# Kernel optimization log

Measured on AMD Instinct MI355X. Metric: run time of the kernel, lower is better.

The kernel has to match this reference:

```python
import jax, jax.numpy as jnp
import numpy as np
from jax import lax

GAMMA = 0.1  # fixed RBF bandwidth from LearnableRBFInfluence


def setup_inputs() -> dict:
    key = jax.random.key(0)
    k1, k2, k3, k4 = jax.random.split(key, 4)
    B, H, W = 2, 256, 256
    NUM_FILTERS, KS, NUM_BASIS = 48, 7, 31
    u_log = jax.random.normal(k1, (B, 1, H, W), jnp.float32)
    f_log = jax.random.normal(k2, (B, 1, H, W), jnp.float32)
    filters = jax.random.normal(k3, (NUM_FILTERS, 1, KS, KS), jnp.float32) * 0.05
    rbf_weights = jax.random.normal(k4, (NUM_FILTERS, NUM_BASIS), jnp.float32) * 0.05
    lambda_param = jnp.float32(0.1)
    return {"u_log": u_log, "f_log": f_log, "filters": filters,
            "rbf_weights": rbf_weights, "lambda_param": lambda_param}


def reference(u_log, f_log, filters, rbf_weights, lambda_param):
    # Batched form of the per-filter loop:
    #   conv[i] = conv2d(u, k_i)  ->  one grouped conv with 48 output channels
    num_basis = rbf_weights.shape[1]
    mu = jnp.linspace(-1.0, 1.0, num_basis).astype(u_log.dtype)  # [K]

    dn = lax.conv_dimension_numbers(u_log.shape, filters.shape, ('NCHW', 'OIHW', 'NCHW'))
    conv = lax.conv_general_dilated(u_log, filters, (1, 1), 'SAME',
                                    dimension_numbers=dn)  # [B,48,H,W]

    # RBF influence, per filter channel c: phi = sum_k w[c,k] * exp(-(conv-mu_k)^2/(2 g^2))
    diff = conv[..., None] - mu                              # [B,48,H,W,K]
    rbf = jnp.exp(-(diff * diff) / (2.0 * GAMMA * GAMMA))
    phi = jnp.einsum('bchwk,ck->bchw', rbf, rbf_weights)     # [B,48,H,W]

    # Per-filter conv2d(phi_i, flip(k_i)) summed over i == single conv
    # with OIHW weight [1,48,7,7] built from spatially-flipped filters.
    kT = jnp.flip(filters, axis=(2, 3)).transpose(1, 0, 2, 3)  # [1,48,7,7]
    dn2 = lax.conv_dimension_numbers(phi.shape, kT.shape, ('NCHW', 'OIHW', 'NCHW'))
    diffusion = lax.conv_general_dilated(phi, kT, (1, 1), 'SAME',
                                         dimension_numbers=dn2)  # [B,1,H,W]

    reaction = lambda_param * (u_log - f_log)
    return u_log - diffusion - reaction
```

## Files before the change

kernel.cpp:

```cpp
#include <hip/hip_runtime.h>

#define HH 256
#define WW 256
#define NPIX (2 * HH * WW)
#define NC 48
#define NB 31
#define NG 6
#define CG 8
#define OT 32
#define PT 38
#define PSTR 44
#define UT 44
#define USTR 52
#define TP 192

__global__ __launch_bounds__(256)
void tnrd_table(const float* __restrict__ wr, float2* __restrict__ tab)
{
    const int ch = blockIdx.x;
    const float* rc = wr + ch * NB;
    for (int j = threadIdx.x; j < TP; j += 256) {
        float v0 = 0.f, v1 = 0.f;
        float x0 = fmaf((float)j, 1.0f / 64.0f, -1.5f);
        float x1 = x0 + 1.0f / 64.0f;
        #pragma unroll
        for (int k = 0; k < NB; ++k) {
            float mu = -1.f + (float)k * (1.f / 15.f);
            float d0 = x0 - mu, d1 = x1 - mu;
            float w = rc[k];
            v0 = fmaf(w, __expf(-50.f * d0 * d0), v0);
            v1 = fmaf(w, __expf(-50.f * d1 * d1), v1);
        }
        tab[ch * TP + j] = make_float2(v0, v1 - v0);
    }
}

__global__ __launch_bounds__(256, 3)
void tnrd_main(const float* __restrict__ u,
               const float* __restrict__ wf,
               const float2* __restrict__ tab,
               float* __restrict__ part)
{
    __shared__ __align__(16) float u_s[UT * USTR];
    __shared__ __align__(16) float phi_s[4][PT * PSTR];

    const int tid = threadIdx.x;
    const int bx = blockIdx.x, by = blockIdx.y;
    const int b = blockIdx.z / NG, g = blockIdx.z % NG;
    const int c0g = g * CG;

    const int uy0 = by * OT - 6, ux0 = bx * OT - 6;
    const float* ub = u + b * (HH * WW);
    for (int i = tid; i < UT * USTR; i += 256) {
        int r = i / USTR, c = i - r * USTR;
        int gy = uy0 + r, gx = ux0 + c;
        float v = 0.f;
        if (c < UT && (unsigned)gy < HH && (unsigned)gx < WW)
            v = ub[gy * WW + gx];
        u_s[i] = v;
    }
    __syncthreads();

    const int oy = tid >> 3;
    const int ox0 = (tid & 7) * 4;
    float o0 = 0.f, o1 = 0.f, o2 = 0.f, o3 = 0.f;
    const int py0 = by * OT - 3, px0 = bx * OT - 3;

    auto conv1_pass = [&](int cp, float* __restrict__ bufA,
                          float* __restrict__ bufB) {
        const float* wA = wf + (c0g + 2 * cp) * 49;
        const float* wB = wA + 49;
        const float2* tA = tab + (c0g + 2 * cp) * TP;
        const float2* tB = tA + TP;
        for (int p = 0; p < 2; ++p) {
            const int gi = tid + p * 256;
            if (gi < PT * 10) {
                const int pr = gi % PT, pc = (gi / PT) * 4;
                float a0 = 0.f, a1 = 0.f, a2 = 0.f, a3 = 0.f;
                float b0 = 0.f, b1 = 0.f, b2 = 0.f, b3 = 0.f;
                const float* bptr = &u_s[pr * USTR + pc];

                auto fmab = [&](const float* wa, const float* wb,
                                float4 q0, float4 q1, float4 q2) {
                    float sv[12] = {q0.x, q0.y, q0.z, q0.w,
                                    q1.x, q1.y, q1.z, q1.w,
                                    q2.x, q2.y, q2.z, q2.w};
                    #pragma unroll
                    for (int dx = 0; dx < 7; ++dx) {
                        float fa = wa[dx], fb = wb[dx];
                        a0 = fmaf(sv[dx],     fa, a0);
                        a1 = fmaf(sv[dx + 1], fa, a1);
                        a2 = fmaf(sv[dx + 2], fa, a2);
                        a3 = fmaf(sv[dx + 3], fa, a3);
                        b0 = fmaf(sv[dx],     fb, b0);
                        b1 = fmaf(sv[dx + 1], fb, b1);
                        b2 = fmaf(sv[dx + 2], fb, b2);
                        b3 = fmaf(sv[dx + 3], fb, b3);
                    }
                };

                float4 c0 = *(const float4*)(bptr);
                float4 c1 = *(const float4*)(bptr + 4);
                float4 c2 = *(const float4*)(bptr + 8);
                #pragma unroll 1
                for (int dy = 0; dy < 6; ++dy) {
                    const float* nr = bptr + (dy + 1) * USTR;
                    float4 n0 = *(const float4*)(nr);
                    float4 n1 = *(const float4*)(nr + 4);
                    float4 n2 = *(const float4*)(nr + 8);
                    fmab(wA + dy * 7, wB + dy * 7, c0, c1, c2);
                    c0 = n0; c1 = n1; c2 = n2;
                }
                fmab(wA + 42, wB + 42, c0, c1, c2);

                const int gy = py0 + pr;
                const bool rowok = (unsigned)gy < HH;
                float av[4] = {a0, a1, a2, a3};
                float bv[4] = {b0, b1, b2, b3};
                float pha[4], phb[4];
                #pragma unroll
                for (int j = 0; j < 4; ++j) {
                    bool ok = rowok && (unsigned)(px0 + pc + j) < WW;
                    float ta = fminf(fmaxf(fmaf(av[j], 64.f, 96.f), 0.f), 191.999f);
                    float fja = floorf(ta);
                    float2 ea = tA[(int)fja];
                    float va = fmaf(ta - fja, ea.y, ea.x);
                    float tb = fminf(fmaxf(fmaf(bv[j], 64.f, 96.f), 0.f), 191.999f);
                    float fjb = floorf(tb);
                    float2 eb = tB[(int)fjb];
                    float vb = fmaf(tb - fjb, eb.y, eb.x);
                    pha[j] = ok ? va : 0.f;
                    phb[j] = ok ? vb : 0.f;
                }
                float* dA = bufA + pr * PSTR + pc;
                float* dB = bufB + pr * PSTR + pc;
                #pragma unroll
                for (int j = 0; j < 4; ++j) dA[j] = pha[j];
                #pragma unroll
                for (int j = 0; j < 4; ++j) dB[j] = phb[j];
            }
        }
    };

    conv1_pass(0, phi_s[0], phi_s[1]);
    __syncthreads();

    #pragma unroll 1
    for (int pass = 0; pass < 4; ++pass) {
        if (pass < 3) {
            const int nb_ = (pass + 1) & 1;
            conv1_pass(pass + 1, phi_s[2 * nb_], phi_s[2 * nb_ + 1]);
        }

        const float* wA = wf + (c0g + 2 * pass) * 49;
        const float* wB = wA + 49;
        const float* pA = phi_s[2 * (pass & 1)];
        const float* pB = phi_s[2 * (pass & 1) + 1];
        for (int dy = 0; dy < 7; ++dy) {
            const float* rA = pA + (oy + dy) * PSTR + ox0;
            const float* rB = pB + (oy + dy) * PSTR + ox0;
            float sa[10], sb[10];
            #pragma unroll
            for (int j = 0; j < 10; ++j) sa[j] = rA[j];
            #pragma unroll
            for (int j = 0; j < 10; ++j) sb[j] = rB[j];
            #pragma unroll
            for (int dx = 0; dx < 7; ++dx) {
                float fa = wA[(6 - dy) * 7 + (6 - dx)];
                float fb = wB[(6 - dy) * 7 + (6 - dx)];
                o0 = fmaf(sa[dx],     fa, o0);
                o1 = fmaf(sa[dx + 1], fa, o1);
                o2 = fmaf(sa[dx + 2], fa, o2);
                o3 = fmaf(sa[dx + 3], fa, o3);
                o0 = fmaf(sb[dx],     fb, o0);
                o1 = fmaf(sb[dx + 1], fb, o1);
                o2 = fmaf(sb[dx + 2], fb, o2);
                o3 = fmaf(sb[dx + 3], fb, o3);
            }
        }
        if (pass < 3) __syncthreads();
    }

    const int gy = by * OT + oy, gx = bx * OT + ox0;
    float4 v4 = make_float4(o0, o1, o2, o3);
    *reinterpret_cast<float4*>(part + (size_t)g * NPIX + b * (HH * WW)
                               + gy * WW + gx) = v4;
}

__global__ __launch_bounds__(256)
void combine_kernel(const float* __restrict__ u,
                    const float* __restrict__ f,
                    const float* __restrict__ lam,
                    const float* __restrict__ part,
                    float* __restrict__ out)
{
    int i = blockIdx.x * 256 + threadIdx.x;
    float d = 0.f;
    #pragma unroll
    for (int g = 0; g < NG; ++g) d += part[g * NPIX + i];
    float lv = lam[0];
    float uv = u[i];
    float fv = f[i];
    out[i] = uv - d - lv * (uv - fv);
}

extern "C" void kernel_launch(void* const* d_in, const int* in_sizes, int n_in,
                              void* d_out, int out_size, void* d_ws, size_t ws_size,
                              hipStream_t stream) {
    const float* u    = (const float*)d_in[0];
    const float* f    = (const float*)d_in[1];
    const float* filt = (const float*)d_in[2];
    const float* rbfw = (const float*)d_in[3];
    const float* lam  = (const float*)d_in[4];
    float* out = (float*)d_out;
    float* part = (float*)d_ws;
    float2* tabg = (float2*)d_out;

    tnrd_table<<<NC, 256, 0, stream>>>(rbfw, tabg);
    tnrd_main<<<dim3(8, 8, 2 * NG), 256, 0, stream>>>(u, filt, tabg, part);
    combine_kernel<<<512, 256, 0, stream>>>(u, f, lam, part, out);
}
```

Before: 110.5 us.

## Fuse RBF table build into main kernel with LDS table and vectorized LDS loads

Removes the separate table kernel launch. Each block now builds the RBF lookup table for its 8 channels in shared memory, using phi_s as scratch, and the LERP lookups read from LDS instead of global memory. The conv1 and conv2 inner loops are rewritten with float4/float2 LDS loads and manually unrolled macros, with vectorized float4 stores of phi. The cost is redundant table computation in every block (768 blocks each doing roughly 1544 points times 31 exps) and extra LDS usage that may reduce occupancy.

```diff
diff --git a/kernel.cpp b/kernel.cpp
--- a/kernel.cpp
+++ b/kernel.cpp
@@ -14,35 +14,46 @@
 #define USTR 52
 #define TP 192
 
-__global__ __launch_bounds__(256)
-void tnrd_table(const float* __restrict__ wr, float2* __restrict__ tab)
-{
-    const int ch = blockIdx.x;
-    const float* rc = wr + ch * NB;
-    for (int j = threadIdx.x; j < TP; j += 256) {
-        float v0 = 0.f, v1 = 0.f;
-        float x0 = fmaf((float)j, 1.0f / 64.0f, -1.5f);
-        float x1 = x0 + 1.0f / 64.0f;
-        #pragma unroll
-        for (int k = 0; k < NB; ++k) {
-            float mu = -1.f + (float)k * (1.f / 15.f);
-            float d0 = x0 - mu, d1 = x1 - mu;
-            float w = rc[k];
-            v0 = fmaf(w, __expf(-50.f * d0 * d0), v0);
-            v1 = fmaf(w, __expf(-50.f * d1 * d1), v1);
-        }
-        tab[ch * TP + j] = make_float2(v0, v1 - v0);
-    }
-}
+
+#define F1STEP(WI, s0, s1, s2, s3)                                      \
+    { float fa = wa[WI], fb = wb[WI];                                   \
+      a0 = fmaf(s0, fa, a0); a1 = fmaf(s1, fa, a1);                     \
+      a2 = fmaf(s2, fa, a2); a3 = fmaf(s3, fa, a3);                     \
+      b0 = fmaf(s0, fb, b0); b1 = fmaf(s1, fb, b1);                     \
+      b2 = fmaf(s2, fb, b2); b3 = fmaf(s3, fb, b3); }
+
+#define F1ROW(WA, WB, q0, q1, q2)                                       \
+    { const float* wa = (WA); const float* wb = (WB);                   \
+      F1STEP(0, q0.x, q0.y, q0.z, q0.w)                                 \
+      F1STEP(1, q0.y, q0.z, q0.w, q1.x)                                 \
+      F1STEP(2, q0.z, q0.w, q1.x, q1.y)                                 \
+      F1STEP(3, q0.w, q1.x, q1.y, q1.z)                                 \
+      F1STEP(4, q1.x, q1.y, q1.z, q1.w)                                 \
+      F1STEP(5, q1.y, q1.z, q1.w, q2.x)                                 \
+      F1STEP(6, q1.z, q1.w, q2.x, q2.y) }
+
+#define LERP1(res, aval, T)                                             \
+    { float t_ = fminf(fmaxf(fmaf(aval, 64.f, 96.f), 0.f), 191.999f);   \
+      float fj_ = floorf(t_);                                           \
+      float2 e_ = (T)[(int)fj_];                       \
+      res = fmaf(t_ - fj_, e_.y, e_.x); }
+
+#define C2STEP(WI, s0, s1, s2, s3, t0, t1, t2, t3)                      \
+    { float fa = wra[WI], fb = wrb[WI];                                 \
+      o0 = fmaf(s0, fa, o0); o1 = fmaf(s1, fa, o1);                     \
+      o2 = fmaf(s2, fa, o2); o3 = fmaf(s3, fa, o3);                     \
+      o0 = fmaf(t0, fb, o0); o1 = fmaf(t1, fb, o1);                     \
+      o2 = fmaf(t2, fb, o2); o3 = fmaf(t3, fb, o3); }
 
 __global__ __launch_bounds__(256, 3)
 void tnrd_main(const float* __restrict__ u,
                const float* __restrict__ wf,
-               const float2* __restrict__ tab,
+               const float* __restrict__ wr,
                float* __restrict__ part)
 {
     __shared__ __align__(16) float u_s[UT * USTR];
     __shared__ __align__(16) float phi_s[4][PT * PSTR];
+    __shared__ __align__(16) float2 tabs[CG][TP];
 
     const int tid = threadIdx.x;
     const int bx = blockIdx.x, by = blockIdx.y;
@@ -59,6 +70,28 @@
             v = ub[gy * WW + gx];
         u_s[i] = v;
     }
+
+    float* tv = &phi_s[0][0];
+    for (int i = tid; i < CG * (TP + 1); i += 256) {
+        int ch = i / (TP + 1), j = i - ch * (TP + 1);
+        const float* rc = wr + (c0g + ch) * NB;
+        float x = fmaf((float)j, 1.0f / 64.0f, -1.5f);
+        float v = 0.f;
+        #pragma unroll
+        for (int k = 0; k < NB; ++k) {
+            float mu = -1.f + (float)k * (1.f / 15.f);
+            float d = x - mu;
+            v = fmaf(rc[k], __expf(-50.f * d * d), v);
+        }
+        tv[i] = v;
+    }
+    __syncthreads();
+    for (int i = tid; i < CG * TP; i += 256) {
+        int ch = i / TP, j = i - ch * TP;
+        float v0 = tv[ch * (TP + 1) + j];
+        float v1 = tv[ch * (TP + 1) + j + 1];
+        tabs[ch][j] = make_float2(v0, v1 - v0);
+    }
     __syncthreads();
 
     const int oy = tid >> 3;
@@ -70,8 +103,8 @@
                           float* __restrict__ bufB) {
         const float* wA = wf + (c0g + 2 * cp) * 49;
         const float* wB = wA + 49;
-        const float2* tA = tab + (c0g + 2 * cp) * TP;
-        const float2* tB = tA + TP;
+        const float2* tA = tabs[2 * cp];
+        const float2* tB = tabs[2 * cp + 1];
         for (int p = 0; p < 2; ++p) {
             const int gi = tid + p * 256;
             if (gi < PT * 10) {
@@ -80,64 +113,39 @@
                 float b0 = 0.f, b1 = 0.f, b2 = 0.f, b3 = 0.f;
                 const float* bptr = &u_s[pr * USTR + pc];
 
-                auto fmab = [&](const float* wa, const float* wb,
-                                float4 q0, float4 q1, float4 q2) {
-                    float sv[12] = {q0.x, q0.y, q0.z, q0.w,
-                                    q1.x, q1.y, q1.z, q1.w,
-                                    q2.x, q2.y, q2.z, q2.w};
-                    #pragma unroll
-                    for (int dx = 0; dx < 7; ++dx) {
-                        float fa = wa[dx], fb = wb[dx];
-                        a0 = fmaf(sv[dx],     fa, a0);
-                        a1 = fmaf(sv[dx + 1], fa, a1);
-                        a2 = fmaf(sv[dx + 2], fa, a2);
-                        a3 = fmaf(sv[dx + 3], fa, a3);
-                        b0 = fmaf(sv[dx],     fb, b0);
-                        b1 = fmaf(sv[dx + 1], fb, b1);
-                        b2 = fmaf(sv[dx + 2], fb, b2);
-                        b3 = fmaf(sv[dx + 3], fb, b3);
-                    }
-                };
-
                 float4 c0 = *(const float4*)(bptr);
                 float4 c1 = *(const float4*)(bptr + 4);
-                float4 c2 = *(const float4*)(bptr + 8);
+                float2 c2 = *(const float2*)(bptr + 8);
                 #pragma unroll 1
                 for (int dy = 0; dy < 6; ++dy) {
                     const float* nr = bptr + (dy + 1) * USTR;
                     float4 n0 = *(const float4*)(nr);
                     float4 n1 = *(const float4*)(nr + 4);
-                    float4 n2 = *(const float4*)(nr + 8);
-                    fmab(wA + dy * 7, wB + dy * 7, c0, c1, c2);
+                    float2 n2 = *(const float2*)(nr + 8);
+                    F1ROW(wA + dy * 7, wB + dy * 7, c0, c1, c2)
                     c0 = n0; c1 = n1; c2 = n2;
                 }
-                fmab(wA + 42, wB + 42, c0, c1, c2);
+                F1ROW(wA + 42, wB + 42, c0, c1, c2)
 
                 const int gy = py0 + pr;
                 const bool rowok = (unsigned)gy < HH;
-                float av[4] = {a0, a1, a2, a3};
-                float bv[4] = {b0, b1, b2, b3};
-                float pha[4], phb[4];
-                #pragma unroll
-                for (int j = 0; j < 4; ++j) {
-                    bool ok = rowok && (unsigned)(px0 + pc + j) < WW;
-                    float ta = fminf(fmaxf(fmaf(av[j], 64.f, 96.f), 0.f), 191.999f);
-                    float fja = floorf(ta);
-                    float2 ea = tA[(int)fja];
-                    float va = fmaf(ta - fja, ea.y, ea.x);
-                    float tb = fminf(fmaxf(fmaf(bv[j], 64.f, 96.f), 0.f), 191.999f);
-                    float fjb = floorf(tb);
-                    float2 eb = tB[(int)fjb];
-                    float vb = fmaf(tb - fjb, eb.y, eb.x);
-                    pha[j] = ok ? va : 0.f;
-                    phb[j] = ok ? vb : 0.f;
-                }
-                float* dA = bufA + pr * PSTR + pc;
-                float* dB = bufB + pr * PSTR + pc;
-                #pragma unroll
-                for (int j = 0; j < 4; ++j) dA[j] = pha[j];
-                #pragma unroll
-                for (int j = 0; j < 4; ++j) dB[j] = phb[j];
+                const bool ok0 = rowok && (unsigned)(px0 + pc + 0) < WW;
+                const bool ok1 = rowok && (unsigned)(px0 + pc + 1) < WW;
+                const bool ok2 = rowok && (unsigned)(px0 + pc + 2) < WW;
+                const bool ok3 = rowok && (unsigned)(px0 + pc + 3) < WW;
+                float pA0, pA1, pA2, pA3, pB0, pB1, pB2, pB3;
+                LERP1(pA0, a0, tA) LERP1(pB0, b0, tB)
+                LERP1(pA1, a1, tA) LERP1(pB1, b1, tB)
+                LERP1(pA2, a2, tA) LERP1(pB2, b2, tB)
+                LERP1(pA3, a3, tA) LERP1(pB3, b3, tB)
+                pA0 = ok0 ? pA0 : 0.f;  pB0 = ok0 ? pB0 : 0.f;
+                pA1 = ok1 ? pA1 : 0.f;  pB1 = ok1 ? pB1 : 0.f;
+                pA2 = ok2 ? pA2 : 0.f;  pB2 = ok2 ? pB2 : 0.f;
+                pA3 = ok3 ? pA3 : 0.f;  pB3 = ok3 ? pB3 : 0.f;
+                *(float4*)(bufA + pr * PSTR + pc) =
+                    make_float4(pA0, pA1, pA2, pA3);
+                *(float4*)(bufB + pr * PSTR + pc) =
+                    make_float4(pB0, pB1, pB2, pB3);
             }
         }
     };
@@ -159,24 +167,21 @@
         for (int dy = 0; dy < 7; ++dy) {
             const float* rA = pA + (oy + dy) * PSTR + ox0;
             const float* rB = pB + (oy + dy) * PSTR + ox0;
-            float sa[10], sb[10];
-            #pragma unroll
-            for (int j = 0; j < 10; ++j) sa[j] = rA[j];
-            #pragma unroll
-            for (int j = 0; j < 10; ++j) sb[j] = rB[j];
-            #pragma unroll
-            for (int dx = 0; dx < 7; ++dx) {
-                float fa = wA[(6 - dy) * 7 + (6 - dx)];
-                float fb = wB[(6 - dy) * 7 + (6 - dx)];
-                o0 = fmaf(sa[dx],     fa, o0);
-                o1 = fmaf(sa[dx + 1], fa, o1);
-                o2 = fmaf(sa[dx + 2], fa, o2);
-                o3 = fmaf(sa[dx + 3], fa, o3);
-                o0 = fmaf(sb[dx],     fb, o0);
-                o1 = fmaf(sb[dx + 1], fb, o1);
-                o2 = fmaf(sb[dx + 2], fb, o2);
-                o3 = fmaf(sb[dx + 3], fb, o3);
-            }
+            const float4 A0 = *(const float4*)(rA);
+            const float4 A1 = *(const float4*)(rA + 4);
+            const float2 A2 = *(const float2*)(rA + 8);
+            const float4 B0 = *(const float4*)(rB);
+            const float4 B1 = *(const float4*)(rB + 4);
+            const float2 B2 = *(const float2*)(rB + 8);
+            const float* wra = wA + (6 - dy) * 7;
+            const float* wrb = wB + (6 - dy) * 7;
+            C2STEP(6, A0.x, A0.y, A0.z, A0.w, B0.x, B0.y, B0.z, B0.w)
+            C2STEP(5, A0.y, A0.z, A0.w, A1.x, B0.y, B0.z, B0.w, B1.x)
+            C2STEP(4, A0.z, A0.w, A1.x, A1.y, B0.z, B0.w, B1.x, B1.y)
+            C2STEP(3, A0.w, A1.x, A1.y, A1.z, B0.w, B1.x, B1.y, B1.z)
+            C2STEP(2, A1.x, A1.y, A1.z, A1.w, B1.x, B1.y, B1.z, B1.w)
+            C2STEP(1, A1.y, A1.z, A1.w, A2.x, B1.y, B1.z, B1.w, B2.x)
+            C2STEP(0, A1.z, A1.w, A2.x, A2.y, B1.z, B1.w, B2.x, B2.y)
         }
         if (pass < 3) __syncthreads();
     }
@@ -214,9 +219,7 @@
     const float* lam  = (const float*)d_in[4];
     float* out = (float*)d_out;
     float* part = (float*)d_ws;
-    float2* tabg = (float2*)d_out;
-
-    tnrd_table<<<NC, 256, 0, stream>>>(rbfw, tabg);
-    tnrd_main<<<dim3(8, 8, 2 * NG), 256, 0, stream>>>(u, filt, tabg, part);
+
+    tnrd_main<<<dim3(8, 8, 2 * NG), 256, 0, stream>>>(u, filt, rbfw, part);
     combine_kernel<<<512, 256, 0, stream>>>(u, f, lam, part, out);
 }
```

Result: slower. 114.7 us (+3.9%).
